# Kernel optimization log

Measured on AMD Instinct MI355X. Metric: run time of the kernel, lower is better.

## Reference

```python
import jax, jax.numpy as jnp
import numpy as np

B, S, D, T = 512, 65536, 256, 10   # graphs, substructures, emb_dim, num_tasks
THRESHOLD = 0.4                    # CausalGNN threshold default
MEMBER_P = 0.002                   # ~131 substructures per graph


def setup_inputs() -> dict:
    key = jax.random.key(0)
    ks = jax.random.split(key, 8)
    def w(k, shape):
        fan_in = shape[0]
        return jax.random.normal(k, shape, jnp.float32) / np.float32(np.sqrt(fan_in))
    return {
        "h_graph": jax.random.normal(ks[0], (B, D), jnp.float32),
        "h_sub":   jax.random.normal(ks[1], (S, D), jnp.float32),
        "W1": w(ks[2], (D, 2 * D)),  "b1": jnp.zeros((2 * D,), jnp.float32),
        "W2": w(ks[3], (2 * D, 1)),  "b2": jnp.zeros((1,), jnp.float32),
        "Wc": w(ks[4], (2 * D, T)),  "bc": jnp.zeros((T,), jnp.float32),
        # dense [B,S] bool membership: mask[i,j] = substructure j belongs to graph i
        "mask": jax.random.bernoulli(ks[5], MEMBER_P, (B, S)),
    }


def _l2_normalize(x, eps=1e-12):  # F.normalize(p=2, dim=1)
    n = jnp.linalg.norm(x, axis=1, keepdims=True)
    return x / jnp.maximum(n, eps)


def reference(h_graph, h_sub, W1, b1, W2, b2, Wc, bc, mask):
    # SubMaskGenerator: Linear -> ReLU -> Dropout(eval=identity) -> Linear -> sigmoid, squeeze
    gate_logits = (jax.nn.relu(h_sub @ W1 + b1) @ W2 + b2)[:, 0]      # [S]
    subgraph_mask = jax.nn.sigmoid(gate_logits)                        # [S]

    # fused masked segment mean (replaces per-graph python loop + host sync):
    # valid[i,j] = (sub j in graph i) & (gate > threshold)
    valid = mask & (subgraph_mask > THRESHOLD)                         # [B,S] bool
    w = valid.astype(h_sub.dtype)
    counts = w.sum(axis=1, keepdims=True)                              # [B,1]
    sums = w @ h_sub                                                   # [B,D]
    h_sub_aligned = jnp.where(counts > 0, sums / jnp.maximum(counts, 1.0), 0.0)

    h_sub_norm = _l2_normalize(h_sub_aligned)
    h_graph_norm = _l2_normalize(h_graph)
    # F.cosine_similarity(dim=1, eps=1e-8) on the already-normalized vectors
    na = jnp.linalg.norm(h_sub_norm, axis=1)
    ng = jnp.linalg.norm(h_graph_norm, axis=1)
    cos = (h_sub_norm * h_graph_norm).sum(axis=1) / (
        jnp.maximum(na, 1e-8) * jnp.maximum(ng, 1e-8))
    cosine_loss = 1.0 - cos.mean()

    h_combined = jnp.concatenate([h_graph, h_sub_aligned], axis=1)     # [B,2D]
    logits = h_combined @ Wc + bc                                      # [B,T]
    return logits, cosine_loss, subgraph_mask
```

## Files before the change

### kernel.cpp

```cpp
#include <hip/hip_runtime.h>
#include <math.h>

#define D 256
#define H 512
#define TT 10
#define THRESH 0.4f
#define KS 8
#define NSPLIT 16

typedef __attribute__((ext_vector_type(8))) _Float16 half8;
typedef __attribute__((ext_vector_type(4))) float f32x4;

__global__ __launch_bounds__(256) void w1_prep(const float* __restrict__ W1,
                                               short* __restrict__ W1s)
{
    const int tid = blockIdx.x * 256 + threadIdx.x;
    const int lane = tid & 63;
    const int cell = tid >> 6;
    const int k = cell & 7;
    const int n = cell >> 3;
    const int row0 = k * 32 + (lane >> 4) * 8;
    const int col = n * 16 + (lane & 15);
    _Float16 h8[8];
    #pragma unroll
    for (int i = 0; i < 8; ++i)
        h8[i] = (_Float16)W1[(size_t)(row0 + i) * H + col];
    *reinterpret_cast<half8*>(W1s + (((size_t)n * 8 + k) * 64 + lane) * 8) =
        *reinterpret_cast<half8*>(h8);
}

__global__ __launch_bounds__(256, 4) void gate_mfma(
    const float* __restrict__ h_sub,
    const short* __restrict__ W1s,
    const float* __restrict__ b1,
    const float* __restrict__ W2,
    const float* __restrict__ b2,
    float* __restrict__ submask,
    unsigned* __restrict__ gbits)
{
    __shared__ __align__(16) short sB[2][8192];
    __shared__ float sb1[H], sw2[H];
    const int tid = threadIdx.x;
    const int lane = tid & 63;
    const int w = tid >> 6;
    const int base = blockIdx.x * 128 + w * 32;
    const int rot = blockIdx.x & 15;
    const float bb = b2[0];

    auto stage = [&](int cc, int b) {
        const int c = (cc + rot) & 15;
        const char* gp = (const char*)W1s + ((size_t)c << 14) + (size_t)tid * 16;
        char* lp0 = (char*)&sB[b][0] + (size_t)tid * 16;
        #pragma unroll
        for (int i = 0; i < 4; ++i) {
            __builtin_amdgcn_global_load_lds(
                (const __attribute__((address_space(1))) void*)(gp + i * 4096),
                (__attribute__((address_space(3))) void*)(lp0 + i * 4096),
                16, 0, 0);
        }
    };

    stage(0, 0);
    stage(1, 1);

    {
        int i = tid * 2;
        *reinterpret_cast<float2*>(&sb1[i]) = *reinterpret_cast<const float2*>(&b1[i]);
        *reinterpret_cast<float2*>(&sw2[i]) = *reinterpret_cast<const float2*>(&W2[i]);
    }

    half8 af[2][KS];
    #pragma unroll
    for (int s = 0; s < 2; ++s) {
        const int row = base + s * 16 + (lane & 15);
        const float* rp = h_sub + (size_t)row * D + (lane >> 4) * 8;
        #pragma unroll
        for (int k = 0; k < KS; ++k) {
            float x[8];
            *reinterpret_cast<float4*>(&x[0]) =
                *reinterpret_cast<const float4*>(rp + k * 32);
            *reinterpret_cast<float4*>(&x[4]) =
                *reinterpret_cast<const float4*>(rp + k * 32 + 4);
            _Float16 h8[8];
            #pragma unroll
            for (int i = 0; i < 8; ++i) h8[i] = (_Float16)x[i];
            af[s][k] = *reinterpret_cast<half8*>(h8);
        }
    }

    __syncthreads();

    float lp[2][4] = {{0.f,0.f,0.f,0.f},{0.f,0.f,0.f,0.f}};

    for (int cc = 0; cc < 16; ++cc) {
        if (cc < 15) asm volatile("s_waitcnt vmcnt(4)" ::: "memory");
        else         asm volatile("s_waitcnt vmcnt(0)" ::: "memory");
        __builtin_amdgcn_s_barrier();
        __builtin_amdgcn_sched_barrier(0);

        const short* buf = &sB[cc & 1][0];
        const int c = (cc + rot) & 15;

        f32x4 acc[2][2];
        #pragma unroll
        for (int s = 0; s < 2; ++s)
            #pragma unroll
            for (int nt = 0; nt < 2; ++nt)
                acc[s][nt] = (f32x4){0.f,0.f,0.f,0.f};

        __builtin_amdgcn_s_setprio(1);
        #pragma unroll
        for (int k = 0; k < KS; ++k) {
            half8 bh0 = *reinterpret_cast<const half8*>(buf + ((0 * 8 + k) * 64 + lane) * 8);
            half8 bh1 = *reinterpret_cast<const half8*>(buf + ((1 * 8 + k) * 64 + lane) * 8);
            acc[0][0] = __builtin_amdgcn_mfma_f32_16x16x32_f16(af[0][k], bh0, acc[0][0], 0, 0, 0);
            acc[1][0] = __builtin_amdgcn_mfma_f32_16x16x32_f16(af[1][k], bh0, acc[1][0], 0, 0, 0);
            acc[0][1] = __builtin_amdgcn_mfma_f32_16x16x32_f16(af[0][k], bh1, acc[0][1], 0, 0, 0);
            acc[1][1] = __builtin_amdgcn_mfma_f32_16x16x32_f16(af[1][k], bh1, acc[1][1], 0, 0, 0);
        }
        __builtin_amdgcn_s_setprio(0);

        #pragma unroll
        for (int nt = 0; nt < 2; ++nt) {
            const int hc = c * 32 + nt * 16 + (lane & 15);
            const float b1h = sb1[hc], w2h = sw2[hc];
            #pragma unroll
            for (int s = 0; s < 2; ++s)
                #pragma unroll
                for (int j = 0; j < 4; ++j) {
                    float v = acc[s][nt][j] + b1h;
                    v = v > 0.f ? v : 0.f;
                    lp[s][j] = fmaf(v, w2h, lp[s][j]);
                }
        }

        __builtin_amdgcn_sched_barrier(0);
        __builtin_amdgcn_s_barrier();
        if (cc < 14) stage(cc + 2, cc & 1);
    }

    #pragma unroll
    for (int m = 1; m < 16; m <<= 1)
        #pragma unroll
        for (int s = 0; s < 2; ++s)
            #pragma unroll
            for (int j = 0; j < 4; ++j)
                lp[s][j] += __shfl_xor(lp[s][j], m);

    const int g = lane >> 4;
    unsigned bits = 0;
    float sig[2][4];
    #pragma unroll
    for (int s = 0; s < 2; ++s)
        #pragma unroll
        for (int j = 0; j < 4; ++j) {
            sig[s][j] = 1.f / (1.f + expf(-(lp[s][j] + bb)));
            if (sig[s][j] > THRESH) bits |= 1u << (s * 16 + g * 4 + j);
        }
    bits |= __shfl_xor(bits, 16);
    bits |= __shfl_xor(bits, 32);
    if (lane == 0) gbits[blockIdx.x * 4 + w] = bits;

    if ((lane & 15) == 0)
        #pragma unroll
        for (int s = 0; s < 2; ++s)
            #pragma unroll
            for (int j = 0; j < 4; ++j)
                submask[base + s * 16 + g * 4 + j] = sig[s][j];
}

__global__ __launch_bounds__(256) void seg_scan(
    const float* __restrict__ h_sub,
    const int*   __restrict__ mask,
    const unsigned* __restrict__ gbits,
    float* __restrict__ psum,
    int*   __restrict__ pcnt,
    int S)
{
    const int i = blockIdx.x / NSPLIT;
    const int p = blockIdx.x % NSPLIT;
    const int tid = threadIdx.x;
    const int lane = tid & 63;
    const int w = tid >> 6;
    const int seg = S / NSPLIT;
    const int start = p * seg;
    const int* mrow = mask + (size_t)i * S + start;

    __shared__ unsigned sbits[4096 / 32];
    if (tid < seg / 32) sbits[tid] = gbits[(start >> 5) + tid];

    const int wbase = w * 1024;
    int4 m4[4];
    #pragma unroll
    for (int it = 0; it < 4; ++it)
        m4[it] = *reinterpret_cast<const int4*>(mrow + wbase + it * 256 + (lane << 2));

    __syncthreads();

    float4 acc = make_float4(0.f, 0.f, 0.f, 0.f);
    int cnt = 0;

    #pragma unroll
    for (int it = 0; it < 4; ++it) {
        const int j0 = wbase + it * 256 + (lane << 2);
        const unsigned bw = sbits[j0 >> 5];
        const int sh = j0 & 31;
        unsigned long long bal[4];
        bal[0] = __ballot((m4[it].x != 0) & ((bw >> (sh + 0)) & 1u));
        bal[1] = __ballot((m4[it].y != 0) & ((bw >> (sh + 1)) & 1u));
        bal[2] = __ballot((m4[it].z != 0) & ((bw >> (sh + 2)) & 1u));
        bal[3] = __ballot((m4[it].w != 0) & ((bw >> (sh + 3)) & 1u));
        #pragma unroll
        for (int s = 0; s < 4; ++s) {
            unsigned long long b = bal[s];
            while (b) {
                int t = __builtin_ctzll(b);
                b &= b - 1;
                int jj = start + wbase + it * 256 + (t << 2) + s;
                float4 hv = *reinterpret_cast<const float4*>(
                    h_sub + (size_t)jj * D + (lane << 2));
                acc.x += hv.x; acc.y += hv.y; acc.z += hv.z; acc.w += hv.w;
                cnt++;
            }
        }
    }

    __shared__ float ssum[4][D];
    __shared__ int   scnt[4];
    *reinterpret_cast<float4*>(&ssum[w][lane << 2]) = acc;
    if (lane == 0) scnt[w] = cnt;
    __syncthreads();

    float a = ssum[0][tid] + ssum[1][tid] + ssum[2][tid] + ssum[3][tid];
    psum[(size_t)blockIdx.x * D + tid] = a;
    if (tid == 0) pcnt[blockIdx.x] = scnt[0] + scnt[1] + scnt[2] + scnt[3];
}

__global__ __launch_bounds__(256) void seg_combine(
    const float* __restrict__ h_graph,
    const float* __restrict__ psum,
    const int*   __restrict__ pcnt,
    const float* __restrict__ Wc,
    const float* __restrict__ bc,
    float* __restrict__ logits,
    float* __restrict__ cos_ws)
{
    const int i = blockIdx.x;
    const int tid = threadIdx.x;
    const int lane = tid & 63;
    const int w = tid >> 6;

    float a = 0.f;
    int c = 0;
    #pragma unroll
    for (int p = 0; p < NSPLIT; ++p) {
        a += psum[((size_t)i * NSPLIT + p) * D + tid];
        c += pcnt[i * NSPLIT + p];
    }
    a = (c > 0) ? (a / (float)c) : 0.f;
    const float g = h_graph[(size_t)i * D + tid];

    float r0 = a * a, r1 = g * g, r2 = a * g;
    #pragma unroll
    for (int m = 1; m < 64; m <<= 1) {
        r0 += __shfl_xor(r0, m);
        r1 += __shfl_xor(r1, m);
        r2 += __shfl_xor(r2, m);
    }
    __shared__ float red[4][3];
    if (lane == 0) { red[w][0] = r0; red[w][1] = r1; red[w][2] = r2; }
    __syncthreads();
    if (tid == 0) {
        float a2 = red[0][0] + red[1][0] + red[2][0] + red[3][0];
        float g2 = red[0][1] + red[1][1] + red[2][1] + red[3][1];
        float ag = red[0][2] + red[1][2] + red[2][2] + red[3][2];
        float an = sqrtf(a2), gn = sqrtf(g2);
        float cs = (c > 0) ? (ag / (fmaxf(an, 1e-12f) * fmaxf(gn, 1e-12f))) : 0.f;
        cos_ws[i] = cs;
    }

    float lg[TT];
    #pragma unroll
    for (int t = 0; t < TT; ++t)
        lg[t] = g * Wc[(size_t)tid * TT + t] + a * Wc[(size_t)(D + tid) * TT + t];
    #pragma unroll
    for (int m = 1; m < 64; m <<= 1)
        #pragma unroll
        for (int t = 0; t < TT; ++t) lg[t] += __shfl_xor(lg[t], m);
    __shared__ float lpart[4][TT];
    if (lane == 0)
        #pragma unroll
        for (int t = 0; t < TT; ++t) lpart[w][t] = lg[t];
    __syncthreads();
    if (tid < TT)
        logits[(size_t)i * TT + tid] =
            lpart[0][tid] + lpart[1][tid] + lpart[2][tid] + lpart[3][tid] + bc[tid];
}

__global__ void loss_kernel(const float* __restrict__ cos_ws,
                            float* __restrict__ out, int B)
{
    const int lane = threadIdx.x;
    float s = 0.f;
    for (int i = lane; i < B; i += 64) s += cos_ws[i];
    #pragma unroll
    for (int m = 1; m < 64; m <<= 1) s += __shfl_xor(s, m);
    if (lane == 0) out[0] = 1.0f - s / (float)B;
}

extern "C" void kernel_launch(void* const* d_in, const int* in_sizes, int n_in,
                              void* d_out, int out_size, void* d_ws, size_t ws_size,
                              hipStream_t stream)
{
    const float* h_graph = (const float*)d_in[0];
    const float* h_sub   = (const float*)d_in[1];
    const float* W1      = (const float*)d_in[2];
    const float* b1      = (const float*)d_in[3];
    const float* W2      = (const float*)d_in[4];
    const float* b2      = (const float*)d_in[5];
    const float* Wc      = (const float*)d_in[6];
    const float* bc      = (const float*)d_in[7];
    const int*   mask    = (const int*)d_in[8];

    const int B = in_sizes[0] / D;
    const int S = in_sizes[1] / D;

    float* out     = (float*)d_out;
    float* logits  = out;
    float* loss    = out + (size_t)B * TT;
    float* submask = loss + 1;

    char* ws = (char*)d_ws;
    short*    W1s    = (short*)ws;
    unsigned* gbits  = (unsigned*)(ws + 512 * 1024);
    int*      pcnt   = (int*)(ws + 528 * 1024);
    float*    cos_ws = (float*)(ws + 576 * 1024);
    float*    psum   = (float*)(ws + 1024 * 1024);

    w1_prep<<<64, 256, 0, stream>>>(W1, W1s);
    gate_mfma<<<S / 128, 256, 0, stream>>>(h_sub, W1s, b1, W2, b2, submask, gbits);
    seg_scan<<<B * NSPLIT, 256, 0, stream>>>(h_sub, mask, gbits, psum, pcnt, S);
    seg_combine<<<B, 256, 0, stream>>>(h_graph, psum, pcnt, Wc, bc, logits, cos_ws);
    loss_kernel<<<1, 64, 0, stream>>>(cos_ws, loss, B);
}
```

Before: 72.23 us.

## Compress membership mask to bitmasks inside gate kernel to overlap with MFMA

Adds extra blocks to the gate kernel that read the 128MB int32 membership mask and ballot it into 64-bit bitmasks written to workspace. seg_scan then reads these compact bitmasks instead of the full int mask. The mask streaming runs concurrently with the compute-bound gate MFMA work instead of serially after it. It adds a bitmask write/read round trip, and the gate kernel's launch grows by many extra blocks.

```diff
diff --git a/kernel.cpp b/kernel.cpp
--- a/kernel.cpp
+++ b/kernel.cpp
@@ -7,6 +7,7 @@
 #define THRESH 0.4f
 #define KS 8
 #define NSPLIT 16
+#define NGB 512
 
 typedef __attribute__((ext_vector_type(8))) _Float16 half8;
 typedef __attribute__((ext_vector_type(4))) float f32x4;
@@ -29,20 +30,48 @@
         *reinterpret_cast<half8*>(h8);
 }
 
-__global__ __launch_bounds__(256, 4) void gate_mfma(
+__global__ __launch_bounds__(256, 4) void gate_fused(
     const float* __restrict__ h_sub,
     const short* __restrict__ W1s,
     const float* __restrict__ b1,
     const float* __restrict__ W2,
     const float* __restrict__ b2,
+    const int*   __restrict__ mask,
     float* __restrict__ submask,
-    unsigned* __restrict__ gbits)
+    unsigned* __restrict__ gbits,
+    unsigned long long* __restrict__ cmask)
 {
     __shared__ __align__(16) short sB[2][8192];
     __shared__ float sb1[H], sw2[H];
     const int tid = threadIdx.x;
     const int lane = tid & 63;
     const int w = tid >> 6;
+
+    if (blockIdx.x >= NGB) {
+        const int mb = blockIdx.x - NGB;
+        const int mw = mb * 4 + w;
+        const size_t g0 = (size_t)mw * 32;
+        for (int it = 0; it < 4; ++it) {
+            int4 m4[8];
+            #pragma unroll
+            for (int u = 0; u < 8; ++u)
+                m4[u] = *reinterpret_cast<const int4*>(
+                    mask + (g0 + it * 8 + u) * 256 + (lane << 2));
+            #pragma unroll
+            for (int u = 0; u < 8; ++u) {
+                unsigned long long c0 = __ballot(m4[u].x != 0);
+                unsigned long long c1 = __ballot(m4[u].y != 0);
+                unsigned long long c2 = __ballot(m4[u].z != 0);
+                unsigned long long c3 = __ballot(m4[u].w != 0);
+                if (lane == 0) {
+                    unsigned long long* cp = cmask + (g0 + it * 8 + u) * 4;
+                    cp[0] = c0; cp[1] = c1; cp[2] = c2; cp[3] = c3;
+                }
+            }
+        }
+        return;
+    }
+
     const int base = blockIdx.x * 128 + w * 32;
     const int rot = blockIdx.x & 15;
     const float bb = b2[0];
@@ -171,7 +200,7 @@
 
 __global__ __launch_bounds__(256) void seg_scan(
     const float* __restrict__ h_sub,
-    const int*   __restrict__ mask,
+    const unsigned long long* __restrict__ cmask,
     const unsigned* __restrict__ gbits,
     float* __restrict__ psum,
     int*   __restrict__ pcnt,
@@ -184,17 +213,11 @@
     const int w = tid >> 6;
     const int seg = S / NSPLIT;
     const int start = p * seg;
-    const int* mrow = mask + (size_t)i * S + start;
+    const unsigned long long* cm =
+        cmask + ((size_t)i * (S / 256) + (size_t)p * (seg / 256)) * 4;
 
     __shared__ unsigned sbits[4096 / 32];
     if (tid < seg / 32) sbits[tid] = gbits[(start >> 5) + tid];
-
-    const int wbase = w * 1024;
-    int4 m4[4];
-    #pragma unroll
-    for (int it = 0; it < 4; ++it)
-        m4[it] = *reinterpret_cast<const int4*>(mrow + wbase + it * 256 + (lane << 2));
-
     __syncthreads();
 
     float4 acc = make_float4(0.f, 0.f, 0.f, 0.f);
@@ -202,21 +225,22 @@
 
     #pragma unroll
     for (int it = 0; it < 4; ++it) {
-        const int j0 = wbase + it * 256 + (lane << 2);
+        const int g = w * 4 + it;
+        const int j0 = g * 256 + (lane << 2);
         const unsigned bw = sbits[j0 >> 5];
         const int sh = j0 & 31;
         unsigned long long bal[4];
-        bal[0] = __ballot((m4[it].x != 0) & ((bw >> (sh + 0)) & 1u));
-        bal[1] = __ballot((m4[it].y != 0) & ((bw >> (sh + 1)) & 1u));
-        bal[2] = __ballot((m4[it].z != 0) & ((bw >> (sh + 2)) & 1u));
-        bal[3] = __ballot((m4[it].w != 0) & ((bw >> (sh + 3)) & 1u));
+        bal[0] = __ballot((bw >> (sh + 0)) & 1u) & cm[(size_t)g * 4 + 0];
+        bal[1] = __ballot((bw >> (sh + 1)) & 1u) & cm[(size_t)g * 4 + 1];
+        bal[2] = __ballot((bw >> (sh + 2)) & 1u) & cm[(size_t)g * 4 + 2];
+        bal[3] = __ballot((bw >> (sh + 3)) & 1u) & cm[(size_t)g * 4 + 3];
         #pragma unroll
         for (int s = 0; s < 4; ++s) {
             unsigned long long b = bal[s];
             while (b) {
                 int t = __builtin_ctzll(b);
                 b &= b - 1;
-                int jj = start + wbase + it * 256 + (t << 2) + s;
+                int jj = start + g * 256 + (t << 2) + s;
                 float4 hv = *reinterpret_cast<const float4*>(
                     h_sub + (size_t)jj * D + (lane << 2));
                 acc.x += hv.x; acc.y += hv.y; acc.z += hv.z; acc.w += hv.w;
@@ -336,10 +360,14 @@
     int*      pcnt   = (int*)(ws + 528 * 1024);
     float*    cos_ws = (float*)(ws + 576 * 1024);
     float*    psum   = (float*)(ws + 1024 * 1024);
-
+    unsigned long long* cmask =
+        (unsigned long long*)(ws + 16 * 1024 * 1024);
+
+    const int nMaskBlocks = (B * (S / 256)) / 128;
     w1_prep<<<64, 256, 0, stream>>>(W1, W1s);
-    gate_mfma<<<S / 128, 256, 0, stream>>>(h_sub, W1s, b1, W2, b2, submask, gbits);
-    seg_scan<<<B * NSPLIT, 256, 0, stream>>>(h_sub, mask, gbits, psum, pcnt, S);
+    gate_fused<<<NGB + nMaskBlocks, 256, 0, stream>>>(
+        h_sub, W1s, b1, W2, b2, mask, submask, gbits, cmask);
+    seg_scan<<<B * NSPLIT, 256, 0, stream>>>(h_sub, cmask, gbits, psum, pcnt, S);
     seg_combine<<<B, 256, 0, stream>>>(h_graph, psum, pcnt, Wc, bc, logits, cos_ws);
     loss_kernel<<<1, 64, 0, stream>>>(cos_ws, loss, B);
 }
```

After: 67.80 us. -6.1%, faster.
